# Performance work log

Measured on AMD Instinct MI355X. Metric: run time of the kernel, lower is better.

The kernel has to match this reference:

```python
import jax, jax.numpy as jnp
import numpy as np

B, T, H, N = 1, 256, 32, 128
HN = H * N
KVH = 8
KV_DIM = KVH * N
KV_REPEAT = HN // KV_DIM
ROPE_THETA = 10000.0
EPS = 1e-6
NTK_ALPHA = 10.0
YARN_MAX = 4096.0
LORA_W, LORA_A, LORA_V, LORA_G = 64, 64, 32, 128
LAYER_ID = 1


def t5_rmsnorm(x, w):
    xf = x.astype(jnp.float32)
    var = jnp.mean(xf * xf, axis=-1, keepdims=True)
    return (w * (xf * jax.lax.rsqrt(var + EPS))).astype(x.dtype)


def rotate_half(x):
    h = x.shape[-1] // 2
    return jnp.concatenate([-x[..., h:], x[..., :h]], axis=-1)


def rope_cache(cache_pos, seq_len, rotary_dim):
    # YaRN-style mix of short/long inv_freq, per compute_rope_cache_range
    half = rotary_dim // 2
    fs = jnp.arange(half, dtype=jnp.float32)
    inv_short = 1.0 / ROPE_THETA ** (fs / half)
    inv_long = 1.0 / (ROPE_THETA * NTK_ALPHA ** (fs / half))
    pos = cache_pos.astype(jnp.float32) + jnp.arange(seq_len, dtype=jnp.float32)[None, :]  # [B,T]
    mix = jnp.clip(pos / YARN_MAX, 0.0, 1.0)[..., None]
    freqs = (1.0 - mix) * (pos[..., None] * inv_short) + mix * (pos[..., None] * inv_long)
    emb = jnp.concatenate([freqs, freqs], axis=-1)  # [B,T,rotary_dim]
    return jnp.cos(emb), jnp.sin(emb)


def _forward(x_in, v_first, state, cache_position, w0, w1, w2, a0, a1, a2, v0, v1, v2, g1, g2,
             r_k, R_, K_, V_, O_, R_bias, K_bias, V_bias, ln_r, ln_k, ln1, ln2):
    x = t5_rmsnorm(x_in, ln1)  # [B,T,HN]
    # float path of fpx_matmul: x @ W.T (+ bias), i.e. the dequantized math
    r = x @ R_.T + R_bias
    k = x @ K_.T + K_bias
    v = x @ V_.T + V_bias
    r = t5_rmsnorm(r.reshape(B, T, H, N), ln_r)      # [B,T,H,N]
    k = t5_rmsnorm(k.reshape(B, T, KVH, N), ln_k)    # [B,T,KVH,N]
    cos, sin = rope_cache(cache_position, T, N)      # [B,T,N]
    cos_, sin_ = cos[:, :, None, :], sin[:, :, None, :]
    r = r * cos_ + rotate_half(r) * sin_
    k = k * cos_ + rotate_half(k) * sin_
    # decay lora: w = -softplus(-(tanh(x@w1)@w2 + w0)) - 0.5
    w = jnp.tanh(x @ w1) @ w2 + w0
    w = -jax.nn.softplus(-w) - 0.5
    # GQA repeat_kv: each kv head repeated KV_REPEAT times contiguously
    v = v.reshape(B, T, KVH, N)
    k = jnp.repeat(k, KV_REPEAT, axis=2).reshape(B, T, HN)
    v = jnp.repeat(v, KV_REPEAT, axis=2).reshape(B, T, HN)
    a = jax.nn.sigmoid((x @ a1) @ a2 + a0)
    g = jax.nn.sigmoid(x @ g1) @ g2
    k4 = k.reshape(B, T, H, N)
    kk = (k4 / jnp.maximum(jnp.linalg.norm(k4, axis=-1, keepdims=True), 1e-12)).reshape(B, T, HN)
    k = k * (1.0 - w + a)
    aa = -kk
    bb = kk * a
    if LAYER_ID == 0:
        v_first = v
    else:
        gate = jax.nn.sigmoid((x @ v1) @ v2 + v0)
        v = v + (v_first - v) * gate
    w = -jnp.exp(w.astype(jnp.float32))  # log-decay for the recurrence

    def to_tm(t):  # [B,T,HN] or [B,T,H,N] -> time-major [T,B,H,N]
        return jnp.moveaxis(t.reshape(B, T, H, N), 1, 0)

    rt, wt, kt, vt, at, bt = map(to_tm, (r, w, k, v, aa, bb))

    def step(S, inp):
        # RWKV-7: S = S*diag(exp(w)) + S @ (a b^T) + v k^T ; out = S @ r
        r_t, w_t, k_t, v_t, a_t, b_t = inp
        sa = jnp.einsum('bhij,bhj->bhi', S, a_t)
        S = S * jnp.exp(w_t)[:, :, None, :] + sa[..., None] * b_t[:, :, None, :] + v_t[..., None] * k_t[:, :, None, :]
        return S, jnp.einsum('bhij,bhj->bhi', S, r_t)

    S_final, outs = jax.lax.scan(step, state.astype(jnp.float32), (rt, wt, kt, vt, at, bt))
    xx = jnp.moveaxis(outs, 0, 1).reshape(B, T, HN) * (float(N) ** -0.5)
    bonus = jnp.sum(r.reshape(B, T, H, N) * k.reshape(B, T, H, N) * r_k, axis=-1, keepdims=True) * v.reshape(B, T, H, N)
    xx = xx.astype(r.dtype) + bonus.reshape(B, T, HN)
    x_res = x_in + (xx * g) @ O_.T
    out = t5_rmsnorm(x_res, ln2)
    return out, x[:, -1], S_final, v_first, x_res


def setup_inputs() -> dict:
    key = jax.random.key(0)
    ks = iter(jax.random.split(key, 32))
    rn = lambda *s: jax.random.normal(next(ks), s, dtype=jnp.float32)
    wt = lambda *s: rn(*s) * 0.02
    return dict(
        x_in=rn(B, T, HN),
        v_first=rn(B, T, HN),
        state=jnp.zeros((B, H, N, N), jnp.float32),
        cache_position=jnp.zeros((B, 1), jnp.int32),
        w0=wt(HN), w1=wt(HN, LORA_W), w2=wt(LORA_W, HN),
        a0=wt(HN), a1=wt(HN, LORA_A), a2=wt(LORA_A, HN),
        v0=wt(HN), v1=wt(HN, LORA_V), v2=wt(LORA_V, HN),
        g1=wt(HN, LORA_G), g2=wt(LORA_G, HN),
        r_k=wt(H, N),
        R_=wt(HN, HN), K_=wt(KV_DIM, HN), V_=wt(KV_DIM, HN), O_=wt(HN, HN),
        R_bias=wt(HN), K_bias=wt(KV_DIM), V_bias=wt(KV_DIM),
        ln_r=jnp.ones((N,), jnp.float32), ln_k=jnp.ones((N,), jnp.float32),
        ln1=jnp.ones((HN,), jnp.float32), ln2=jnp.ones((HN,), jnp.float32),
    )


def reference(x_in, v_first, state, cache_position, w0, w1, w2, a0, a1, a2, v0, v1, v2, g1, g2,
              r_k, R_, K_, V_, O_, R_bias, K_bias, V_bias, ln_r, ln_k, ln1, ln2):
    return _forward(x_in, v_first, state, cache_position, w0, w1, w2, a0, a1, a2, v0, v1, v2,
                    g1, g2, r_k, R_, K_, V_, O_, R_bias, K_bias, V_bias, ln_r, ln_k, ln1, ln2)
```

## Files before the change

### kernel.cpp

```cpp
#include <hip/hip_runtime.h>
#include <cstdint>
#include <cstddef>

#define T_ 256
#define HN_ 4096
#define H_ 32
#define N_ 128
#define SR_ 6464

typedef __attribute__((ext_vector_type(8))) short short8;
typedef __attribute__((ext_vector_type(4))) float f32x4;

__device__ __forceinline__ short f2bf(float f) {
    uint32_t u = __builtin_bit_cast(uint32_t, f);
    u = (u + 0x7fffu + ((u >> 16) & 1u)) >> 16;
    return (short)u;
}
__device__ __forceinline__ short f2bfc(float f) {
    return (short)((__builtin_bit_cast(uint32_t, f) + 0x8000u) >> 16);
}
__device__ __forceinline__ short8 cvt8r(float4 lo, float4 hi) {
    short8 v;
    v[0] = f2bfc(lo.x); v[1] = f2bfc(lo.y); v[2] = f2bfc(lo.z); v[3] = f2bfc(lo.w);
    v[4] = f2bfc(hi.x); v[5] = f2bfc(hi.y); v[6] = f2bfc(hi.z); v[7] = f2bfc(hi.w);
    return v;
}
__device__ __forceinline__ f32x4 mfma16(short8 a, short8 b, f32x4 c) {
    return __builtin_amdgcn_mfma_f32_16x16x32_bf16(a, b, c, 0, 0, 0);
}
__device__ __forceinline__ float sigm(float x) { return 1.f / (1.f + expf(-x)); }
__device__ __forceinline__ float splus(float x) { return (x > 20.f) ? x : log1pf(expf(x)); }

__device__ __forceinline__ float bf1(ushort u) {
    return __builtin_bit_cast(float, (uint32_t)u << 16);
}
__device__ __forceinline__ void gload_lds16(const void* g, void* l) {
    __builtin_amdgcn_global_load_lds(
        (const __attribute__((address_space(1))) void*)g,
        (__attribute__((address_space(3))) void*)l, 16, 0, 0);
}

template <int CTRL>
__device__ __forceinline__ float dpp_add(float v) {
    int p = __builtin_amdgcn_mov_dpp(__builtin_bit_cast(int, v), CTRL, 0xF, 0xF, true);
    return v + __builtin_bit_cast(float, p);
}
__device__ __forceinline__ float reduce64(float v) {
    v = dpp_add<0xB1>(v);
    v = dpp_add<0x4E>(v);
    v = dpp_add<0x124>(v);
    v = dpp_add<0x128>(v);
    v = dpp_add<0x142>(v);
    v = dpp_add<0x143>(v);
    int r = __builtin_amdgcn_readlane(__builtin_bit_cast(int, v), 63);
    return __builtin_bit_cast(float, r);
}

__device__ __forceinline__ void gemm_core(
    const ushort* __restrict__ A, const float* __restrict__ Brow,
    int kbeg, float* LB, f32x4 acc[2][2]) {
    const int tid = threadIdx.x, wid = tid >> 6, l = tid & 63;
    const int ar = l & 15, ak = (l >> 4) * 8;
    const int mBase = wid * 32;

    const int p1 = tid, p2 = tid + 512;
    const int r1 = p1 >> 5, c1 = (p1 & 31) ^ (r1 & 7);
    const int r2 = p2 >> 5, c2 = (p2 & 31) ^ (r2 & 7);
    const float* sb1 = Brow + (size_t)r1 * 4096 + kbeg + c1 * 4;
    const float* sb2 = Brow + (size_t)r2 * 4096 + kbeg + c2 * 4;
    float* d1 = LB + wid * 256;
    float* d2 = LB + 2048 + wid * 256;

    const ushort* pa0 = A + (size_t)(mBase + ar) * 4096 + kbeg + ak;
    const ushort* pa1 = pa0 + (size_t)16 * 4096;

    const int rb0 = ar * 128, rb1 = (16 + ar) * 128;
    const int sx = ar & 7;
    const int cb = (l >> 4) * 2;

    short8 Ae[8], Ao[8];

#define STAGEB(s, rb) { \
    gload_lds16(sb1 + (size_t)(s) * 128, d1 + (rb) * 4096); \
    gload_lds16(sb2 + (size_t)(s) * 128, d2 + (rb) * 4096); }

#define LA(B_, s) { \
    B_[0] = *(const short8*)(pa0 + (size_t)(s) * 128);      \
    B_[1] = *(const short8*)(pa1 + (size_t)(s) * 128);      \
    B_[2] = *(const short8*)(pa0 + (size_t)(s) * 128 + 32); \
    B_[3] = *(const short8*)(pa1 + (size_t)(s) * 128 + 32); \
    B_[4] = *(const short8*)(pa0 + (size_t)(s) * 128 + 64); \
    B_[5] = *(const short8*)(pa1 + (size_t)(s) * 128 + 64); \
    B_[6] = *(const short8*)(pa0 + (size_t)(s) * 128 + 96); \
    B_[7] = *(const short8*)(pa1 + (size_t)(s) * 128 + 96); }

#define CKK(kk, B_, Lb_) { \
    const int cc = (kk) * 8 + cb; \
    float4 l0 = *(const float4*)(Lb_ + rb0 + ((cc ^ sx) * 4)); \
    float4 h0 = *(const float4*)(Lb_ + rb0 + (((cc + 1) ^ sx) * 4)); \
    float4 l1 = *(const float4*)(Lb_ + rb1 + ((cc ^ sx) * 4)); \
    float4 h1 = *(const float4*)(Lb_ + rb1 + (((cc + 1) ^ sx) * 4)); \
    short8 b0 = cvt8r(l0, h0), b1 = cvt8r(l1, h1); \
    acc[0][0] = mfma16(B_[2 * (kk)], b0, acc[0][0]); \
    acc[0][1] = mfma16(B_[2 * (kk)], b1, acc[0][1]); \
    acc[1][0] = mfma16(B_[2 * (kk) + 1], b0, acc[1][0]); \
    acc[1][1] = mfma16(B_[2 * (kk) + 1], b1, acc[1][1]); }

#define COMPUTE(rb, B_) { const float* Lb_ = LB + (rb) * 4096; \
    CKK(0, B_, Lb_) CKK(1, B_, Lb_) CKK(2, B_, Lb_) CKK(3, B_, Lb_) }

    STAGEB(0, 0)
    LA(Ae, 0)
    STAGEB(1, 1)

    for (int su = 0; su < 4; su++) {
        const int s0 = su * 2, s1 = su * 2 + 1;
        LA(Ao, (s0 + 1 < 8) ? s0 + 1 : 7)
        STAGEB((s0 + 2 < 8) ? s0 + 2 : 7, (s0 + 2) % 3)
        asm volatile("s_waitcnt vmcnt(12)" ::: "memory");
        __builtin_amdgcn_s_barrier();
        __builtin_amdgcn_sched_barrier(0);
        COMPUTE(s0 % 3, Ae)
        __builtin_amdgcn_s_barrier();

        LA(Ae, (s1 + 1 < 8) ? s1 + 1 : 7)
        STAGEB((s1 + 2 < 8) ? s1 + 2 : 7, (s1 + 2) % 3)
        asm volatile("s_waitcnt vmcnt(12)" ::: "memory");
        __builtin_amdgcn_s_barrier();
        __builtin_amdgcn_sched_barrier(0);
        COMPUTE(s1 % 3, Ao)
        __builtin_amdgcn_s_barrier();
    }
    asm volatile("s_waitcnt vmcnt(0)" ::: "memory");
#undef STAGEB
#undef LA
#undef CKK
#undef COMPUTE
}

__global__ __launch_bounds__(256) void rmsnorm_k(const float* __restrict__ in,
                                                 const float* __restrict__ w,
                                                 float* __restrict__ outF,
                                                 ushort* __restrict__ outB,
                                                 float* __restrict__ lastrow) {
    int t = blockIdx.x, tid = threadIdx.x;
    const float4* in4 = (const float4*)(in + (size_t)t * HN_);
    const float4* w4 = (const float4*)w;
    float4 v[4]; float ss = 0.f;
#pragma unroll
    for (int q = 0; q < 4; q++) {
        v[q] = in4[q * 256 + tid];
        ss += v[q].x * v[q].x + v[q].y * v[q].y + v[q].z * v[q].z + v[q].w * v[q].w;
    }
#pragma unroll
    for (int o = 32; o; o >>= 1) ss += __shfl_down(ss, o);
    __shared__ float red[4];
    if ((tid & 63) == 0) red[tid >> 6] = ss;
    __syncthreads();
    float tot = red[0] + red[1] + red[2] + red[3];
    float sc = rsqrtf(tot * (1.f / HN_) + 1e-6f);
#pragma unroll
    for (int q = 0; q < 4; q++) {
        float4 wv = w4[q * 256 + tid];
        float4 r;
        r.x = wv.x * v[q].x * sc; r.y = wv.y * v[q].y * sc;
        r.z = wv.z * v[q].z * sc; r.w = wv.w * v[q].w * sc;
        int idx = q * 256 + tid;
        if (outF) ((float4*)(outF + (size_t)t * HN_))[idx] = r;
        if (outB) {
            ushort4 b;
            b.x = (ushort)f2bf(r.x); b.y = (ushort)f2bf(r.y);
            b.z = (ushort)f2bf(r.z); b.w = (ushort)f2bf(r.w);
            ((ushort4*)(outB + (size_t)t * HN_))[idx] = b;
        }
        if (lastrow && t == T_ - 1) ((float4*)lastrow)[idx] = r;
    }
}

__global__ __launch_bounds__(512, 2) void gemm_rkvt(
    const ushort* __restrict__ A,
    const float* __restrict__ Rw, const float* __restrict__ Kw,
    const float* __restrict__ Vw, const float* __restrict__ WT,
    float* __restrict__ COMB) {
    __shared__ __align__(16) float LB[12288];
    const int tid = threadIdx.x, wid = tid >> 6, l = tid & 63;
    const int mBase = wid * 32;
    const int nB = blockIdx.x * 32;
    const int kbeg = blockIdx.y * 1024;

    const float* Bp; int brow;
    if (nB < 4096)      { Bp = Rw; brow = nB; }
    else if (nB < 5120) { Bp = Kw; brow = nB - 4096; }
    else if (nB < 6144) { Bp = Vw; brow = nB - 5120; }
    else                { Bp = WT; brow = nB - 6144; }

    f32x4 acc[2][2];
#pragma unroll
    for (int i = 0; i < 2; i++)
#pragma unroll
        for (int j = 0; j < 2; j++) acc[i][j] = f32x4{0.f, 0.f, 0.f, 0.f};

    gemm_core(A, Bp + (size_t)brow * 4096, kbeg, LB, acc);

    const int rl = (l >> 4) * 4, cl = l & 15;
#pragma unroll
    for (int mf = 0; mf < 2; mf++)
#pragma unroll
        for (int nf = 0; nf < 2; nf++)
#pragma unroll
            for (int e = 0; e < 4; e++)
                unsafeAtomicAdd(&COMB[(size_t)(mBase + mf * 16 + rl + e) * SR_ + nB + nf * 16 + cl],
                                acc[mf][nf][e]);
}

__global__ __launch_bounds__(512, 2) void gemm_o(
    const ushort* __restrict__ A,
    const float* __restrict__ B,
    float* __restrict__ C) {
    __shared__ __align__(16) float LB[12288];
    const int tid = threadIdx.x, wid = tid >> 6, l = tid & 63;
    const int mBase = wid * 32;
    const int nB = blockIdx.x * 32;
    const int kbeg = blockIdx.y * 1024;

    f32x4 acc[2][2];
#pragma unroll
    for (int i = 0; i < 2; i++)
#pragma unroll
        for (int j = 0; j < 2; j++) acc[i][j] = f32x4{0.f, 0.f, 0.f, 0.f};

    gemm_core(A, B + (size_t)nB * 4096, kbeg, LB, acc);

    const int rl = (l >> 4) * 4, cl = l & 15;
#pragma unroll
    for (int mf = 0; mf < 2; mf++)
#pragma unroll
        for (int nf = 0; nf < 2; nf++)
#pragma unroll
            for (int e = 0; e < 4; e++)
                unsafeAtomicAdd(&C[(size_t)(mBase + mf * 16 + rl + e) * 4096 + nB + nf * 16 + cl],
                                acc[mf][nf][e]);
}

__global__ __launch_bounds__(512) void gemm_s2(
    const ushort* __restrict__ TCB,
    const float* __restrict__ w2, const float* __restrict__ a2,
    const float* __restrict__ v2, const float* __restrict__ g2,
    const float* __restrict__ w0, const float* __restrict__ a0,
    const float* __restrict__ v0,
    float* __restrict__ WPRE, float* __restrict__ APRE,
    float* __restrict__ VGPRE, float* __restrict__ GARR) {
    const int z = blockIdx.y;
    int Aoff, K; const float* B; const float* bias; float* out;
    if (z == 0)      { Aoff = 0;   K = 64;  B = w2; bias = w0;      out = WPRE; }
    else if (z == 1) { Aoff = 64;  K = 64;  B = a2; bias = a0;      out = APRE; }
    else if (z == 2) { Aoff = 128; K = 32;  B = v2; bias = v0;      out = VGPRE; }
    else             { Aoff = 160; K = 128; B = g2; bias = nullptr; out = GARR; }

    const int tid = threadIdx.x, wid = tid >> 6, l = tid & 63;
    const int ar = l & 15, ak = (l >> 4) * 8;
    const int mBase = wid * 32;
    const int nB = blockIdx.x * 32;

    f32x4 acc[2][2];
#pragma unroll
    for (int i = 0; i < 2; i++)
#pragma unroll
        for (int j = 0; j < 2; j++) acc[i][j] = f32x4{0.f, 0.f, 0.f, 0.f};

    for (int k0 = 0; k0 < K; k0 += 32) {
        const ushort* pA = TCB + (size_t)(mBase + ar) * 320 + Aoff + k0 + ak;
        short8 av0 = *(const short8*)pA;
        short8 av1 = *(const short8*)(pA + (size_t)16 * 320);
        short8 bv0, bv1;
#pragma unroll
        for (int e = 0; e < 8; e++) {
            bv0[e] = f2bfc(B[(size_t)(k0 + ak + e) * 4096 + nB + ar]);
            bv1[e] = f2bfc(B[(size_t)(k0 + ak + e) * 4096 + nB + 16 + ar]);
        }
        acc[0][0] = mfma16(av0, bv0, acc[0][0]);
        acc[0][1] = mfma16(av0, bv1, acc[0][1]);
        acc[1][0] = mfma16(av1, bv0, acc[1][0]);
        acc[1][1] = mfma16(av1, bv1, acc[1][1]);
    }
    const int rl = (l >> 4) * 4, cl = l & 15;
#pragma unroll
    for (int mf = 0; mf < 2; mf++)
#pragma unroll
        for (int nf = 0; nf < 2; nf++) {
            int col = nB + nf * 16 + cl;
            float bv = bias ? bias[col] : 0.f;
#pragma unroll
            for (int e = 0; e < 4; e++)
                out[(size_t)(mBase + mf * 16 + rl + e) * 4096 + col] = acc[mf][nf][e] + bv;
        }
}

__global__ __launch_bounds__(256) void wcat2_k(const float* __restrict__ w1p,
                                               const float* __restrict__ a1p,
                                               const float* __restrict__ v1p,
                                               const float* __restrict__ g1p,
                                               float* __restrict__ WT) {
    const int kb = blockIdx.x * 64, tile = blockIdx.y;
    const float* src; int ldw, jo, nb, W;
    if (tile == 0)      { src = w1p; ldw = 64;  jo = 0;  nb = 0;   W = 64; }
    else if (tile == 1) { src = a1p; ldw = 64;  jo = 0;  nb = 64;  W = 64; }
    else if (tile == 2) { src = v1p; ldw = 32;  jo = 0;  nb = 128; W = 32; }
    else if (tile == 3) { src = g1p; ldw = 128; jo = 0;  nb = 160; W = 64; }
    else                { src = g1p; ldw = 128; jo = 64; nb = 224; W = 64; }
    __shared__ float lds[64][65];
    const int ti = threadIdx.x & 63, wi = threadIdx.x >> 6;
    if (ti < W)
        for (int i = wi; i < 64; i += 4)
            lds[i][ti] = src[(size_t)(kb + i) * ldw + jo + ti];
    __syncthreads();
    for (int i2 = wi; i2 < W; i2 += 4)
        WT[(size_t)(nb + i2) * 4096 + kb + ti] = lds[ti][i2];
}

__global__ __launch_bounds__(256) void init_comb_k(const float* __restrict__ Rb,
                                                   const float* __restrict__ Kb,
                                                   const float* __restrict__ Vb,
                                                   float* __restrict__ COMB) {
    int t = blockIdx.x;
    for (int c = threadIdx.x; c < SR_; c += 256) {
        float b = (c < 4096) ? Rb[c] : (c < 5120) ? Kb[c - 4096]
                : (c < 6144) ? Vb[c - 5120] : 0.f;
        COMB[(size_t)t * SR_ + c] = b;
    }
}

__global__ __launch_bounds__(256) void act_k(const float* __restrict__ COMB,
                                             ushort* __restrict__ TCB) {
    int idx = blockIdx.x * 256 + threadIdx.x;
    if (idx >= 256 * 288) return;
    int t = idx / 288, c = idx % 288;
    float v = COMB[(size_t)t * SR_ + 6144 + c];
    if (c < 64) v = tanhf(v);
    else if (c >= 160) v = sigm(v);
    TCB[t * 320 + c] = (ushort)f2bf(v);
}

__global__ __launch_bounds__(256) void prep_k(
    const float* __restrict__ COMB, const float* __restrict__ wpre,
    const float* __restrict__ apre, const float* __restrict__ vgpre,
    const float* __restrict__ vfirst, const float* __restrict__ garr,
    const float* __restrict__ rkg, const int* __restrict__ cpos,
    const float* __restrict__ lnr, const float* __restrict__ lnk,
    ushort* __restrict__ SFB) {
    const int tp = blockIdx.x, hg = blockIdx.y;
    const int tid = threadIdx.x;
    const int w = tid >> 6, lane = tid & 63;
    const int t0 = tp * 2, t1 = t0 + 1;

    float e = (float)lane * (1.f / 64.f);
    float inv_s = exp2f(-13.287712379549449f * e);
    float inv_l = exp2f(-13.287712379549449f - 3.321928094887362f * e);
    float base = (float)cpos[0];
    float pos0 = base + (float)t0, pos1 = base + (float)t1;
    float mix0 = fminf(fmaxf(pos0 * (1.f / 4096.f), 0.f), 1.f);
    float mix1 = fminf(fmaxf(pos1 * (1.f / 4096.f), 0.f), 1.f);
    float fr0 = pos0 * ((1.f - mix0) * inv_s + mix0 * inv_l);
    float fr1 = pos1 * ((1.f - mix1) * inv_s + mix1 * inv_l);
    float cA = cosf(fr0), sA = sinf(fr0);
    float cB = cosf(fr1), sB = sinf(fr1);

    float lr0 = lnr[lane], lr1 = lnr[lane + 64];
    float lk0 = lnk[lane], lk1 = lnk[lane + 64];

    for (int hb = hg * 4; hb < hg * 4 + 4; hb++) {
        int h = hb * 4 + w;
        int kv = h >> 2;
        float rk0 = rkg[h * 128 + lane], rk1 = rkg[h * 128 + 64 + lane];

        auto STEPQ = [&](int t, float cc, float ss,
                         float& Rr0, float& Rr1, float& Kf0, float& Kf1,
                         float& Aa0, float& Aa1, float& Bb0, float& Bb1,
                         float& Dd0, float& Dd1, float& Vv0, float& Vv1,
                         float& Gg0, float& Gg1) {
            size_t tS = (size_t)t * SR_;
            float r0 = COMB[tS + h * 128 + lane];
            float r1 = COMB[tS + h * 128 + 64 + lane];
            float sm = reduce64(r0 * r0 + r1 * r1);
            float sc = rsqrtf(sm * (1.f / 128.f) + 1e-6f);
            float rn0 = lr0 * r0 * sc, rn1 = lr1 * r1 * sc;
            Rr0 = rn0 * cc - rn1 * ss; Rr1 = rn1 * cc + rn0 * ss;
            float k0 = COMB[tS + 4096 + kv * 128 + lane];
            float k1 = COMB[tS + 4096 + kv * 128 + 64 + lane];
            float ks = reduce64(k0 * k0 + k1 * k1);
            float ksc = rsqrtf(ks * (1.f / 128.f) + 1e-6f);
            float kn0 = lk0 * k0 * ksc, kn1 = lk1 * k1 * ksc;
            float kr0 = kn0 * cc - kn1 * ss, kr1 = kn1 * cc + kn0 * ss;
            float nr = reduce64(kr0 * kr0 + kr1 * kr1);
            float inv = 1.f / fmaxf(sqrtf(nr), 1e-12f);
            float kk0 = kr0 * inv, kk1 = kr1 * inv;
            int ch0 = h * 128 + lane, ch1 = ch0 + 64;
            size_t tb = (size_t)t * HN_;
            float wv0 = -splus(-wpre[tb + ch0]) - 0.5f;
            float wv1 = -splus(-wpre[tb + ch1]) - 0.5f;
            Dd0 = expf(-expf(wv0)); Dd1 = expf(-expf(wv1));
            float av0 = sigm(apre[tb + ch0]);
            float av1 = sigm(apre[tb + ch1]);
            float vg0 = sigm(vgpre[tb + ch0]);
            float vg1 = sigm(vgpre[tb + ch1]);
            float vr0 = COMB[tS + 5120 + kv * 128 + lane];
            float vr1 = COMB[tS + 5120 + kv * 128 + 64 + lane];
            Vv0 = vr0 + (vfirst[tb + ch0] - vr0) * vg0;
            Vv1 = vr1 + (vfirst[tb + ch1] - vr1) * vg1;
            Kf0 = kr0 * (1.f - wv0 + av0); Kf1 = kr1 * (1.f - wv1 + av1);
            Aa0 = -kk0; Aa1 = -kk1;
            Bb0 = kk0 * av0; Bb1 = kk1 * av1;
            Gg0 = garr[tb + ch0]; Gg1 = garr[tb + ch1];
        };

        float r00, r01, k00, k01, a00, a01, b00, b01, d00, d01, v00, v01, g00, g01;
        float r10, r11, k10, k11, a10, a11, b10, b11, d10, d11, v10, v11, g10, g11;
        STEPQ(t0, cA, sA, r00, r01, k00, k01, a00, a01, b00, b01, d00, d01, v00, v01, g00, g01);
        STEPQ(t1, cB, sB, r10, r11, k10, k11, a10, a11, b10, b11, d10, d11, v10, v11, g10, g11);

        float* rf = (float*)(SFB + ((size_t)h * 128 + tp) * 3072);
        rf[0    + lane] = a00;        rf[0    + 64 + lane] = a01;
        rf[128  + lane] = d00 * a10;  rf[128  + 64 + lane] = d01 * a11;
        rf[256  + lane] = d00 * r00;  rf[256  + 64 + lane] = d01 * r01;
        rf[384  + lane] = r10;        rf[384  + 64 + lane] = r11;
        rf[512  + lane] = d00 * d10;  rf[512  + 64 + lane] = d01 * d11;
        rf[640  + lane] = b00 * d10;  rf[640  + 64 + lane] = b01 * d11;
        rf[768  + lane] = k00 * d10;  rf[768  + 64 + lane] = k01 * d11;
        rf[896  + lane] = b10;        rf[896  + 64 + lane] = b11;
        rf[1024 + lane] = k10;        rf[1024 + 64 + lane] = k11;
        ushort* us = (ushort*)rf;
        us[2304 + lane] = (ushort)f2bf(v00); us[2304 + 64 + lane] = (ushort)f2bf(v01);
        us[2432 + lane] = (ushort)f2bf(v10); us[2432 + 64 + lane] = (ushort)f2bf(v11);
        us[2560 + lane] = (ushort)f2bf(g00); us[2560 + 64 + lane] = (ushort)f2bf(g01);
        us[2688 + lane] = (ushort)f2bf(g10); us[2688 + 64 + lane] = (ushort)f2bf(g11);

        float C1  = reduce64(b00 * a10 + b01 * a11);
        float C2  = reduce64(k00 * a10 + k01 * a11);
        float C3  = reduce64(b00 * r00 + b01 * r01);
        float C4  = reduce64(k00 * r00 + k01 * r01);
        float BD0 = reduce64(r00 * k00 * rk0 + r01 * k01 * rk1);
        float BD1 = reduce64(r10 * k10 * rk0 + r11 * k11 * rk1);
        if (lane == 0) {
            rf[1408] = C1; rf[1409] = C2; rf[1410] = C3;
            rf[1411] = C4; rf[1412] = BD0; rf[1413] = BD1;
        }
    }
}

#define SDP_ 5
#define SNBP_ 6
__global__ __launch_bounds__(512) void scan_k(
    const float* __restrict__ state_in,
    const ushort* __restrict__ SFB,
    ushort* __restrict__ yb, float* __restrict__ Sout) {
    const int h = blockIdx.x, sp = blockIdx.y;
    const int tid = threadIdx.x;
    const int wv = tid >> 6, ln = tid & 63;
    const int i = sp * 8 + wv;
    const int j0 = ln * 2;

    float S0, S1;
    {
        float2 s2 = *(const float2*)(state_in + ((size_t)h * 128 + i) * 128 + j0);
        S0 = s2.x; S1 = s2.y;
    }

    __shared__ __align__(16) ushort lds_s[SNBP_][3072];
    __shared__ float ybuf[3][16];
    const ushort* hbase = SFB + (size_t)h * 128 * 3072;

    auto STAGE = [&](int buf, int tp) {
        if (wv < 6) {
            const ushort* src = hbase + (size_t)(tp & 127) * 3072 + wv * 512 + ln * 8;
            gload_lds16(src, &lds_s[buf][wv * 512]);
        }
    };

#pragma unroll
    for (int d = 0; d < SDP_; d++) STAGE(d, d);

    float r1c0 = 0.f, r1c1 = 0.f, bd1c = 0.f, vi1c = 0.f, gi1c = 0.f;
    for (int Io = 0; Io < 132; Io += 6) {
#pragma unroll
        for (int u = 0; u < 6; u++) {
            const int I = Io + u;
            if (I >= 128) break;
            const int bc = u;
            const int bs = (u + SDP_) % 6;

            if (wv < 6) asm volatile("s_waitcnt vmcnt(4)" ::: "memory");
            __builtin_amdgcn_s_barrier();
            __builtin_amdgcn_sched_barrier(0);
            asm volatile("" ::: "memory");

            STAGE(bs, I + SDP_);

            if (wv == 7 && ln < 16 && I > 1) {
                int pr = I - 2;
                int row = sp * 8 + (ln >> 1);
                int tt = pr * 2 + (ln & 1);
                yb[(size_t)tt * HN_ + h * 128 + row] =
                    (ushort)f2bf(ybuf[(u + 1) % 3][ln]);
            }

            const ushort* L = lds_s[bc];
            const float* Lf = (const float*)L;
            float2 A0 = *(const float2*)(Lf + 0    + j0);
            float2 WA = *(const float2*)(Lf + 128  + j0);
            float2 WR = *(const float2*)(Lf + 256  + j0);
            float2 R1 = *(const float2*)(Lf + 384  + j0);
            float2 W2 = *(const float2*)(Lf + 512  + j0);
            float2 BW = *(const float2*)(Lf + 640  + j0);
            float2 KW = *(const float2*)(Lf + 768  + j0);
            float2 B1 = *(const float2*)(Lf + 896  + j0);
            float2 K1 = *(const float2*)(Lf + 1024 + j0);
            float vi0 = bf1(L[2304 + i]);
            float vi1 = bf1(L[2432 + i]);
            float gi0 = bf1(L[2560 + i]);
            float gi1 = bf1(L[2688 + i]);
            const float* Sc = Lf + 1408;
            float c1 = Sc[0], c2 = Sc[1], c3 = Sc[2], c4 = Sc[3];
            float bd0 = Sc[4], bd1 = Sc[5];

            float up = fmaf(S0, A0.x, S1 * A0.y);
            float pp = fmaf(S0, WA.x, S1 * WA.y);
            float yp = fmaf(S0, WR.x, S1 * WR.y);
            float op = fmaf(S0, r1c0, S1 * r1c1);
            float u_   = reduce64(up);
            float p_   = reduce64(pp);
            float yb0  = reduce64(yp);
            float od1  = reduce64(op);

            if (I > 0) {
                float cp1 = fmaf(od1, 0.08838834764831845f, bd1c * vi1c) * gi1c;
                if (ln == 0) ybuf[(u + 2) % 3][2 * wv + 1] = cp1;
            }

            float sa0 = u_;
            float sa1 = fmaf(sa0, c1, fmaf(vi0, c2, p_));
            float od0 = fmaf(sa0, c3, fmaf(vi0, c4, yb0));
            float cp0 = fmaf(od0, 0.08838834764831845f, bd0 * vi0) * gi0;
            if (ln == 0) ybuf[u % 3][2 * wv] = cp0;

            S0 = fmaf(sa0, BW.x, S0 * W2.x);
            S0 = fmaf(vi0, KW.x, S0);
            S0 = fmaf(sa1, B1.x, S0);
            S0 = fmaf(vi1, K1.x, S0);
            S1 = fmaf(sa0, BW.y, S1 * W2.y);
            S1 = fmaf(vi0, KW.y, S1);
            S1 = fmaf(sa1, B1.y, S1);
            S1 = fmaf(vi1, K1.y, S1);

            r1c0 = R1.x; r1c1 = R1.y;
            bd1c = bd1; vi1c = vi1; gi1c = gi1;
        }
    }

    __builtin_amdgcn_s_barrier();
    {
        float op = fmaf(S0, r1c0, S1 * r1c1);
        float od1 = reduce64(op);
        float cp1 = fmaf(od1, 0.08838834764831845f, bd1c * vi1c) * gi1c;
        if (ln == 0) {
            yb[(size_t)255 * HN_ + h * 128 + i] = (ushort)f2bf(cp1);
            yb[(size_t)254 * HN_ + h * 128 + i] = (ushort)f2bf(ybuf[1][2 * wv]);
            yb[(size_t)252 * HN_ + h * 128 + i] = (ushort)f2bf(ybuf[0][2 * wv]);
            yb[(size_t)253 * HN_ + h * 128 + i] = (ushort)f2bf(ybuf[0][2 * wv + 1]);
        }
    }

    float* pS = Sout + ((size_t)h * 128 + i) * 128 + j0;
    *(float2*)pS = make_float2(S0, S1);
}

extern "C" void kernel_launch(void* const* d_in, const int* in_sizes, int n_in,
                              void* d_out, int out_size, void* d_ws, size_t ws_size,
                              hipStream_t stream) {
    const float* x_in   = (const float*)d_in[0];
    const float* vfirst = (const float*)d_in[1];
    const float* state  = (const float*)d_in[2];
    const int*   cpos   = (const int*)d_in[3];
    const float* w0 = (const float*)d_in[4];
    const float* w1 = (const float*)d_in[5];
    const float* w2 = (const float*)d_in[6];
    const float* a0 = (const float*)d_in[7];
    const float* a1 = (const float*)d_in[8];
    const float* a2 = (const float*)d_in[9];
    const float* v0 = (const float*)d_in[10];
    const float* v1 = (const float*)d_in[11];
    const float* v2 = (const float*)d_in[12];
    const float* g1 = (const float*)d_in[13];
    const float* g2 = (const float*)d_in[14];
    const float* r_k = (const float*)d_in[15];
    const float* R_ = (const float*)d_in[16];
    const float* K_ = (const float*)d_in[17];
    const float* V_ = (const float*)d_in[18];
    const float* O_ = (const float*)d_in[19];
    const float* Rb = (const float*)d_in[20];
    const float* Kb = (const float*)d_in[21];
    const float* Vb = (const float*)d_in[22];
    const float* ln_r = (const float*)d_in[23];
    const float* ln_k = (const float*)d_in[24];
    const float* ln1 = (const float*)d_in[25];
    const float* ln2 = (const float*)d_in[26];

    float* ws = (float*)d_ws;
    constexpr size_t OFF_XB   = 0;
    constexpr size_t OFF_COMB = 524288;
    constexpr size_t OFF_WT   = 2179072;
    constexpr size_t OFF_TCB  = 3489792;
    constexpr size_t OFF_WPRE = 3530752;
    constexpr size_t OFF_APRE = 4579328;
    constexpr size_t OFF_VGPRE= 5627904;
    constexpr size_t OFF_G    = 6676480;
    constexpr size_t OFF_SF   = 7757824;
    constexpr size_t OFF_YB   = OFF_XB;

    ushort* XB  = (ushort*)(ws + OFF_XB);
    float* COMB = ws + OFF_COMB;
    float* WT   = ws + OFF_WT;
    ushort* TCB = (ushort*)(ws + OFF_TCB);
    float* WPRE = ws + OFF_WPRE;
    float* APRE = ws + OFF_APRE;
    float* VGPRE= ws + OFF_VGPRE;
    float* GARR = ws + OFF_G;
    ushort* SFB = (ushort*)(ws + OFF_SF);
    ushort* YB  = (ushort*)(ws + OFF_YB);

    float* out = (float*)d_out;
    float* out0  = out;
    float* xlast = out + 1048576;
    float* Sfin  = out + 1052672;
    float* vfout = out + 1576960;
    float* xres  = out + 2625536;

    hipMemcpyAsync(vfout, vfirst, (size_t)1048576 * 4, hipMemcpyDeviceToDevice, stream);
    hipMemcpyAsync(xres, x_in, (size_t)1048576 * 4, hipMemcpyDeviceToDevice, stream);

    rmsnorm_k<<<T_, 256, 0, stream>>>(x_in, ln1, nullptr, XB, xlast);

    wcat2_k<<<dim3(64, 5), 256, 0, stream>>>(w1, a1, v1, g1, WT);
    hipMemsetAsync(WT + (size_t)288 * 4096, 0, (size_t)32 * 4096 * 4, stream);
    init_comb_k<<<T_, 256, 0, stream>>>(Rb, Kb, Vb, COMB);

    gemm_rkvt<<<dim3(202, 4), 512, 0, stream>>>(XB, R_, K_, V_, WT, COMB);

    act_k<<<288, 256, 0, stream>>>(COMB, TCB);

    gemm_s2<<<dim3(128, 4), 512, 0, stream>>>(TCB, w2, a2, v2, g2, w0, a0, v0,
                                              WPRE, APRE, VGPRE, GARR);

    prep_k<<<dim3(128, 2), 256, 0, stream>>>(COMB, WPRE, APRE, VGPRE, vfirst, GARR,
                                             r_k, cpos, ln_r, ln_k, SFB);

    scan_k<<<dim3(32, 16), 512, 0, stream>>>(state, SFB, YB, Sfin);

    gemm_o<<<dim3(128, 4), 512, 0, stream>>>(YB, O_, xres);

    rmsnorm_k<<<T_, 256, 0, stream>>>(xres, ln2, out0, nullptr, nullptr);
}
```

Measured before the change: 310.6 us.

## Split scan into smaller 4-wave blocks and write outputs directly from registers

```diff
diff --git a/kernel.cpp b/kernel.cpp
--- a/kernel.cpp
+++ b/kernel.cpp
@@ -449,14 +449,15 @@
 
 #define SDP_ 5
 #define SNBP_ 6
-__global__ __launch_bounds__(512) void scan_k(
+__global__ __launch_bounds__(256) void scan_k(
     const float* __restrict__ state_in,
     const ushort* __restrict__ SFB,
-    ushort* __restrict__ yb, float* __restrict__ Sout) {
+    ushort* __restrict__ yb, float* __restrict__ Sout,
+    ushort* __restrict__ dummy) {
     const int h = blockIdx.x, sp = blockIdx.y;
     const int tid = threadIdx.x;
     const int wv = tid >> 6, ln = tid & 63;
-    const int i = sp * 8 + wv;
+    const int i = sp * 4 + wv;
     const int j0 = ln * 2;
 
     float S0, S1;
@@ -466,19 +467,20 @@
     }
 
     __shared__ __align__(16) ushort lds_s[SNBP_][3072];
-    __shared__ float ybuf[3][16];
     const ushort* hbase = SFB + (size_t)h * 128 * 3072;
 
     auto STAGE = [&](int buf, int tp) {
-        if (wv < 6) {
-            const ushort* src = hbase + (size_t)(tp & 127) * 3072 + wv * 512 + ln * 8;
-            gload_lds16(src, &lds_s[buf][wv * 512]);
+        if (wv < 3) {
+            const ushort* src = hbase + (size_t)(tp & 127) * 3072 + wv * 1024 + ln * 8;
+            gload_lds16(src,       &lds_s[buf][wv * 1024]);
+            gload_lds16(src + 512, &lds_s[buf][wv * 1024 + 512]);
         }
     };
 
 #pragma unroll
     for (int d = 0; d < SDP_; d++) STAGE(d, d);
 
+    float pend_y0 = 0.f, pend_y1 = 0.f;
     float r1c0 = 0.f, r1c1 = 0.f, bd1c = 0.f, vi1c = 0.f, gi1c = 0.f;
     for (int Io = 0; Io < 132; Io += 6) {
 #pragma unroll
@@ -488,20 +490,24 @@
             const int bc = u;
             const int bs = (u + SDP_) % 6;
 
-            if (wv < 6) asm volatile("s_waitcnt vmcnt(4)" ::: "memory");
+            if (wv < 3) {
+                if (I < SDP_) asm volatile("s_waitcnt vmcnt(8)" ::: "memory");
+                else          asm volatile("s_waitcnt vmcnt(16)" ::: "memory");
+            }
             __builtin_amdgcn_s_barrier();
             __builtin_amdgcn_sched_barrier(0);
             asm volatile("" ::: "memory");
 
+            if (ln == 0) {
+                ushort* p0 = (I >= 1) ? (yb + (size_t)(2 * I - 2) * HN_ + h * 128 + i)
+                                      : (dummy + tid);
+                *p0 = (ushort)f2bf(pend_y0);
+                ushort* p1 = (I >= 2) ? (yb + (size_t)(2 * I - 3) * HN_ + h * 128 + i)
+                                      : (dummy + 256 + tid);
+                *p1 = (ushort)f2bf(pend_y1);
+            }
+
             STAGE(bs, I + SDP_);
-
-            if (wv == 7 && ln < 16 && I > 1) {
-                int pr = I - 2;
-                int row = sp * 8 + (ln >> 1);
-                int tt = pr * 2 + (ln & 1);
-                yb[(size_t)tt * HN_ + h * 128 + row] =
-                    (ushort)f2bf(ybuf[(u + 1) % 3][ln]);
-            }
 
             const ushort* L = lds_s[bc];
             const float* Lf = (const float*)L;
@@ -531,16 +537,12 @@
             float yb0  = reduce64(yp);
             float od1  = reduce64(op);
 
-            if (I > 0) {
-                float cp1 = fmaf(od1, 0.08838834764831845f, bd1c * vi1c) * gi1c;
-                if (ln == 0) ybuf[(u + 2) % 3][2 * wv + 1] = cp1;
-            }
+            pend_y1 = fmaf(od1, 0.08838834764831845f, bd1c * vi1c) * gi1c;
 
             float sa0 = u_;
             float sa1 = fmaf(sa0, c1, fmaf(vi0, c2, p_));
             float od0 = fmaf(sa0, c3, fmaf(vi0, c4, yb0));
-            float cp0 = fmaf(od0, 0.08838834764831845f, bd0 * vi0) * gi0;
-            if (ln == 0) ybuf[u % 3][2 * wv] = cp0;
+            pend_y0 = fmaf(od0, 0.08838834764831845f, bd0 * vi0) * gi0;
 
             S0 = fmaf(sa0, BW.x, S0 * W2.x);
             S0 = fmaf(vi0, KW.x, S0);
@@ -556,16 +558,14 @@
         }
     }
 
-    __builtin_amdgcn_s_barrier();
     {
         float op = fmaf(S0, r1c0, S1 * r1c1);
         float od1 = reduce64(op);
         float cp1 = fmaf(od1, 0.08838834764831845f, bd1c * vi1c) * gi1c;
         if (ln == 0) {
             yb[(size_t)255 * HN_ + h * 128 + i] = (ushort)f2bf(cp1);
-            yb[(size_t)254 * HN_ + h * 128 + i] = (ushort)f2bf(ybuf[1][2 * wv]);
-            yb[(size_t)252 * HN_ + h * 128 + i] = (ushort)f2bf(ybuf[0][2 * wv]);
-            yb[(size_t)253 * HN_ + h * 128 + i] = (ushort)f2bf(ybuf[0][2 * wv + 1]);
+            yb[(size_t)254 * HN_ + h * 128 + i] = (ushort)f2bf(pend_y0);
+            yb[(size_t)253 * HN_ + h * 128 + i] = (ushort)f2bf(pend_y1);
         }
     }
 
@@ -614,6 +614,7 @@
     constexpr size_t OFF_VGPRE= 5627904;
     constexpr size_t OFF_G    = 6676480;
     constexpr size_t OFF_SF   = 7757824;
+    constexpr size_t OFF_DUM  = 14049280;
     constexpr size_t OFF_YB   = OFF_XB;
 
     ushort* XB  = (ushort*)(ws + OFF_XB);
@@ -625,6 +626,7 @@
     float* VGPRE= ws + OFF_VGPRE;
     float* GARR = ws + OFF_G;
     ushort* SFB = (ushort*)(ws + OFF_SF);
+    ushort* DUM = (ushort*)(ws + OFF_DUM);
     ushort* YB  = (ushort*)(ws + OFF_YB);
 
     float* out = (float*)d_out;
@@ -653,7 +655,7 @@
     prep_k<<<dim3(128, 2), 256, 0, stream>>>(COMB, WPRE, APRE, VGPRE, vfirst, GARR,
                                              r_k, cpos, ln_r, ln_k, SFB);
 
-    scan_k<<<dim3(32, 16), 512, 0, stream>>>(state, SFB, YB, Sfin);
+    scan_k<<<dim3(32, 32), 256, 0, stream>>>(state, SFB, YB, Sfin, DUM);
 
     gemm_o<<<dim3(128, 4), 512, 0, stream>>>(YB, O_, xres);
 
```

After: 308.5 us. About the same (-0.7%).
